# Optimization experiments

Hardware: AMD Instinct MI355X
Metric: run time of the kernel (lower is better)

## Reference

```python
import jax, jax.numpy as jnp
import numpy as np

T_MAX = 0.5
LN_EPS = 1e-5
B, N, D = 256, 16384, 512
NNZ = N * 33  # ~ (2*top_k+1) nonzeros per row of the sparse Laplacian
DF = 4 * D
DT = 32  # time-embedding hidden size


def _layernorm(x, g, b):
    mu = jnp.mean(x, axis=-1, keepdims=True)
    var = jnp.mean((x - mu) ** 2, axis=-1, keepdims=True)
    return (x - mu) * jax.lax.rsqrt(var + LN_EPS) * g + b


def setup_inputs() -> dict:
    key = jax.random.key(0)
    ks = jax.random.split(key, 16)

    def lin_w(k, fan_out, fan_in):
        return jax.random.normal(k, (fan_out, fan_in), jnp.float32) * (1.0 / np.sqrt(fan_in))

    inp = {}
    inp["x0"] = jax.random.uniform(ks[0], (B, N), jnp.float32)
    inp["t"] = jax.random.uniform(ks[1], (B,), jnp.float32)
    inp["L_vals"] = jax.random.normal(ks[2], (NNZ,), jnp.float32) * 0.1
    inp["W_in"] = lin_w(ks[3], D, N)
    inp["b_in"] = jnp.zeros((D,), jnp.float32)
    inp["W_out"] = lin_w(ks[4], N, D)
    inp["b_out"] = jnp.zeros((N,), jnp.float32)
    inp["W_qkv"] = lin_w(ks[5], 3 * D, D)
    inp["b_qkv"] = jnp.zeros((3 * D,), jnp.float32)
    inp["W_o"] = lin_w(ks[6], D, D)
    inp["b_o"] = jnp.zeros((D,), jnp.float32)
    inp["g1"] = jnp.ones((D,), jnp.float32)
    inp["be1"] = jnp.zeros((D,), jnp.float32)
    inp["g2"] = jnp.ones((D,), jnp.float32)
    inp["be2"] = jnp.zeros((D,), jnp.float32)
    inp["W_f1"] = lin_w(ks[7], DF, D)
    inp["b_f1"] = jnp.zeros((DF,), jnp.float32)
    inp["W_f2"] = lin_w(ks[8], D, DF)
    inp["b_f2"] = jnp.zeros((D,), jnp.float32)
    inp["W_t1"] = lin_w(ks[9], DT, 1)
    inp["b_t1"] = jnp.zeros((DT,), jnp.float32)
    inp["W_t2"] = lin_w(ks[10], D, DT)
    inp["b_t2"] = jnp.zeros((D,), jnp.float32)
    inp["L_rows"] = jax.random.randint(ks[11], (NNZ,), 0, N, jnp.int32)
    inp["L_cols"] = jax.random.randint(ks[12], (NNZ,), 0, N, jnp.int32)
    return inp


def reference(x0, t, L_vals, W_in, b_in, W_out, b_out, W_qkv, b_qkv, W_o, b_o,
              g1, be1, g2, be2, W_f1, b_f1, W_f2, b_f2, W_t1, b_t1, W_t2, b_t2,
              L_rows, L_cols):
    n_items = x0.shape[1]
    d_model = W_in.shape[0]
    t_cont = t * T_MAX  # per-sample diffusion time (explicit input, not RNG)

    # Batched sparse Laplacian diffusion (replaces the per-row torch.sparse.mm loop):
    # (L @ x.T)[i, b] = sum_e L_vals[e] * x0[b, L_cols[e]] aggregated to row L_rows[e]
    contrib = x0[:, L_cols] * L_vals                                  # (B, NNZ)
    Lx = jax.ops.segment_sum(contrib.T, L_rows, num_segments=n_items)  # (N, B)
    x_t = x0 - t_cont[:, None] * Lx.T                                  # (B, N)

    # Denoiser (eval mode: dropout off)
    h = x_t @ W_in.T + b_in                                            # (B, D)
    t_norm = t_cont / T_MAX
    te = jax.nn.silu(t_norm[:, None] @ W_t1.T + b_t1) @ W_t2.T + b_t2  # (B, D)
    h = h + te

    # MultiheadAttention on a length-1 sequence: softmax over one key is exactly 1,
    # so attn_out = out_proj(V) with V = h @ W_v.T + b_v.
    qkv = h @ W_qkv.T + b_qkv                                          # (B, 3D)
    v = qkv[:, 2 * d_model:]
    attn_out = v @ W_o.T + b_o

    h = _layernorm(h + attn_out, g1, be1)
    ff = jax.nn.gelu(h @ W_f1.T + b_f1, approximate=False) @ W_f2.T + b_f2
    h = _layernorm(h + ff, g2, be2)

    pred = h @ W_out.T + b_out                                         # (B, N)
    return jnp.mean((pred - x0) ** 2)
```

## Files before the change

### kernel.cpp

```cpp
#include <hip/hip_runtime.h>
#include <math.h>

#define Bb   256
#define Nn   16384
#define Dd   512
#define NNZn 540672
#define DFf  2048
#define SLOT 64

#define CVT_BLKS 4736
#define TR_BLKS  1024
#define BK_BLKS  2112
#define PREP_BLKS (CVT_BLKS + TR_BLKS + BK_BLKS)

#define C1 65536
#define C2 131072
#define C3 393216
#define C4 655360
#define C5 2752512
#define C6 4849664

typedef __bf16 bf16;
typedef __bf16 bf16x4 __attribute__((ext_vector_type(4)));
typedef __bf16 bf16x8 __attribute__((ext_vector_type(8)));
typedef float  f32x4  __attribute__((ext_vector_type(4)));

__device__ __forceinline__ void gload16(const void* g, void* l) {
  __builtin_amdgcn_global_load_lds(
      (const __attribute__((address_space(1))) unsigned int*)g,
      (__attribute__((address_space(3))) unsigned int*)l, 16, 0, 0);
}

template <int NK>
__device__ __forceinline__ void bar_keep() {
  asm volatile("s_waitcnt vmcnt(%0) lgkmcnt(0)" :: "n"(NK) : "memory");
  __builtin_amdgcn_s_barrier();
}

__device__ __forceinline__ float f16_of(unsigned e) {
  unsigned short us = (unsigned short)(e & 0xffff);
  _Float16 h;
  __builtin_memcpy(&h, &us, 2);
  return (float)h;
}

__global__ __launch_bounds__(256) void k_prep(
    const float* __restrict__ w_v, const float* __restrict__ w_o,
    const float* __restrict__ w_f1, const float* __restrict__ w_f2,
    const float* __restrict__ w_in, const float* __restrict__ w_out,
    bf16* __restrict__ o_v, bf16* __restrict__ o_o,
    bf16* __restrict__ o_f1, bf16* __restrict__ o_f2,
    bf16* __restrict__ o_in, bf16* __restrict__ o_out,
    const float* __restrict__ x0, bf16* __restrict__ x0T,
    const int* __restrict__ rows, const int* __restrict__ cols,
    const float* __restrict__ vals,
    int* __restrict__ counts, unsigned* __restrict__ ents,
    float* __restrict__ d_loss) {
  __shared__ float tile[64][65];
  int blk = blockIdx.x;
  if (blk == 0 && threadIdx.x == 0) *d_loss = 0.f;
  int q = blk / 3;
  if ((blk % 3) == 0 && q < BK_BLKS) {
    int i = q * 256 + threadIdx.x;
    int r = rows[i];
    int p = atomicAdd(&counts[r], 1);
    if (p < SLOT) {
      _Float16 hv = (_Float16)vals[i];
      unsigned short us;
      __builtin_memcpy(&us, &hv, 2);
      ents[(size_t)r * SLOT + p] = ((unsigned)cols[i] << 16) | (unsigned)us;
    }
  } else {
    int sB = (blk + 2) / 3; if (sB > BK_BLKS) sB = BK_BLKS;
    int o = blk - sB;
    if (o < CVT_BLKS) {
      int v0i = o * 1024 + threadIdx.x;
#pragma unroll
      for (int j = 0; j < 4; j++) {
        int v = v0i + j * 256;
        const float* s; bf16* d; int base;
        if (v < C2)      { if (v < C1) { s = w_v;  d = o_v;  base = 0;  }
                           else        { s = w_o;  d = o_o;  base = C1; } }
        else if (v < C4) { if (v < C3) { s = w_f1; d = o_f1; base = C2; }
                           else        { s = w_f2; d = o_f2; base = C3; } }
        else             { if (v < C5) { s = w_in; d = o_in; base = C4; }
                           else        { s = w_out; d = o_out; base = C5; } }
        int idx = (v - base) * 4;
        float4 x = *(const float4*)(s + idx);
        bf16x4 ob;
        ob[0] = (bf16)x.x; ob[1] = (bf16)x.y; ob[2] = (bf16)x.z; ob[3] = (bf16)x.w;
        *(bf16x4*)(d + idx) = ob;
      }
    } else {
      int bx = o - CVT_BLKS;
      int n0 = (bx & 255) * 64, b0 = (bx >> 8) * 64;
      int tx = threadIdx.x & 63, ty = threadIdx.x >> 6;
#pragma unroll
      for (int i = 0; i < 16; i++) {
        int bl = ty * 16 + i;
        tile[bl][tx] = x0[(size_t)(b0 + bl) * Nn + n0 + tx];
      }
      __syncthreads();
#pragma unroll
      for (int i = 0; i < 16; i++) {
        int nl = ty * 16 + i;
        x0T[(size_t)(n0 + nl) * Bb + b0 + tx] = (bf16)tile[tx][nl];
      }
    }
  }
}

__global__ __launch_bounds__(256) void k_lx(const bf16x4* __restrict__ x0T4,
                                            const int* __restrict__ counts,
                                            const unsigned* __restrict__ ents,
                                            bf16x4* __restrict__ Lx4) {
  int w = threadIdx.x >> 6, lane = threadIdx.x & 63;
  int r = blockIdx.x * 4 + w;
  __shared__ unsigned esm[4][64];
  int cnt = counts[r];
  if (cnt > SLOT) cnt = SLOT;
  const unsigned* ep = ents + (size_t)r * SLOT;
  float a0 = 0.f, a1 = 0.f, a2 = 0.f, a3 = 0.f;
  float b0 = 0.f, b1 = 0.f, b2 = 0.f, b3 = 0.f;
  float c0 = 0.f, c1 = 0.f, c2 = 0.f, c3 = 0.f;
  float d0 = 0.f, d1 = 0.f, d2 = 0.f, d3 = 0.f;
  for (int base = 0; base < cnt; base += 64) {
    int m = cnt - base; if (m > 64) m = 64;
    if (lane < m) esm[w][lane] = ep[base + lane];
    int i = 0;
    for (; i + 3 < m; i += 4) {
      unsigned e0 = esm[w][i],     e1 = esm[w][i + 1];
      unsigned e2 = esm[w][i + 2], e3 = esm[w][i + 3];
      bf16x4 xv0 = x0T4[(size_t)(e0 >> 16) * 64 + lane];
      bf16x4 xv1 = x0T4[(size_t)(e1 >> 16) * 64 + lane];
      bf16x4 xv2 = x0T4[(size_t)(e2 >> 16) * 64 + lane];
      bf16x4 xv3 = x0T4[(size_t)(e3 >> 16) * 64 + lane];
      float v0 = f16_of(e0), v1 = f16_of(e1), v2 = f16_of(e2), v3 = f16_of(e3);
      a0 += v0 * (float)xv0[0]; a1 += v0 * (float)xv0[1];
      a2 += v0 * (float)xv0[2]; a3 += v0 * (float)xv0[3];
      b0 += v1 * (float)xv1[0]; b1 += v1 * (float)xv1[1];
      b2 += v1 * (float)xv1[2]; b3 += v1 * (float)xv1[3];
      c0 += v2 * (float)xv2[0]; c1 += v2 * (float)xv2[1];
      c2 += v2 * (float)xv2[2]; c3 += v2 * (float)xv2[3];
      d0 += v3 * (float)xv3[0]; d1 += v3 * (float)xv3[1];
      d2 += v3 * (float)xv3[2]; d3 += v3 * (float)xv3[3];
    }
    for (; i < m; i++) {
      unsigned e0 = esm[w][i];
      bf16x4 xv0 = x0T4[(size_t)(e0 >> 16) * 64 + lane];
      float v0 = f16_of(e0);
      a0 += v0 * (float)xv0[0]; a1 += v0 * (float)xv0[1];
      a2 += v0 * (float)xv0[2]; a3 += v0 * (float)xv0[3];
    }
  }
  bf16x4 o;
  o[0] = (bf16)(a0 + b0 + c0 + d0); o[1] = (bf16)(a1 + b1 + c1 + d1);
  o[2] = (bf16)(a2 + b2 + c2 + d2); o[3] = (bf16)(a3 + b3 + c3 + d3);
  Lx4[(size_t)r * 64 + lane] = o;
}

__global__ __launch_bounds__(256) void k_combine(const float* __restrict__ x0,
                                                 const bf16* __restrict__ Lx,
                                                 const float* __restrict__ t,
                                                 bf16* __restrict__ xt) {
  __shared__ float lxs[64][65];
  int n0 = blockIdx.x * 64, b0 = blockIdx.y * 64;
  int tx = threadIdx.x & 63, ty = threadIdx.x >> 6;
#pragma unroll
  for (int i = 0; i < 16; i++) {
    int nl = ty * 16 + i;
    lxs[nl][tx] = (float)Lx[(size_t)(n0 + nl) * Bb + b0 + tx];
  }
  __syncthreads();
#pragma unroll
  for (int i = 0; i < 16; i++) {
    int bl = ty * 16 + i;
    int b  = b0 + bl;
    float tc = t[b] * 0.5f;
    float v = x0[(size_t)b * Nn + n0 + tx] - tc * lxs[tx][bl];
    xt[(size_t)b * Nn + n0 + tx] = (bf16)v;
  }
}

template <int BM, int BN, int MODE, int ACT = 0>
__global__ __launch_bounds__(256) void gemm_tn(
    const bf16* __restrict__ A, const bf16* __restrict__ Bm,
    float* __restrict__ C, int N, int K, int kLen, int MN,
    const float* __restrict__ bias, const float* __restrict__ x0,
    float* __restrict__ lossOut) {
  constexpr int WM = BM / 2, WN = BN / 2, FM = WM / 16, FN = WN / 16;
  constexpr int PASS = (BM + BN) / 64;
  constexpr int KEEP = PASS;
  __shared__ __align__(16) bf16 As[3][BM * 32];
  __shared__ __align__(16) bf16 Bs[3][BN * 32];
  __shared__ float lred[4];
  const int tid = threadIdx.x;
  const int lane = tid & 63, w = tid >> 6;
  const int wm = w >> 1, wn = w & 1;
  const int mBase = blockIdx.x * BM, nBase = blockIdx.y * BN;
  const int k0 = blockIdx.z * kLen;
  const int nIter = kLen >> 5;

  f32x4 acc[FM][FN];
#pragma unroll
  for (int i = 0; i < FM; i++)
#pragma unroll
    for (int j = 0; j < FN; j++) acc[i][j] = {0.f, 0.f, 0.f, 0.f};

  auto stage = [&](int buf, int k) {
#pragma unroll
    for (int p = 0; p < PASS; p++) {
      int c = p * 4 + w;
      int u = c * 64 + lane;
      if (c < BM / 16) {
        int row = u >> 2, sub = u & 3;
        gload16(A + (size_t)(mBase + row) * K + k + sub * 8,
                (char*)As[buf] + c * 1024);
      } else {
        int u2 = u - BM * 4;
        int row = u2 >> 2, sub = u2 & 3;
        gload16(Bm + (size_t)(nBase + row) * K + k + sub * 8,
                (char*)Bs[buf] + (c - BM / 16) * 1024);
      }
    }
  };
  auto compute = [&](int cur) {
    bf16x8 af[FM], bfr[FN];
#pragma unroll
    for (int i = 0; i < FM; i++)
      af[i] = *(const bf16x8*)(As[cur] + (wm * WM + i * 16 + (lane & 15)) * 32 + (lane >> 4) * 8);
#pragma unroll
    for (int j = 0; j < FN; j++)
      bfr[j] = *(const bf16x8*)(Bs[cur] + (wn * WN + j * 16 + (lane & 15)) * 32 + (lane >> 4) * 8);
#pragma unroll
    for (int i = 0; i < FM; i++)
#pragma unroll
      for (int j = 0; j < FN; j++)
        acc[i][j] = __builtin_amdgcn_mfma_f32_16x16x32_bf16(af[i], bfr[j], acc[i][j], 0, 0, 0);
  };

  stage(0, k0);
  if (nIter > 1) {
    stage(1, k0 + 32);
    bar_keep<KEEP>();
  } else {
    bar_keep<0>();
  }

  int c0 = 0, c1 = 1, c2 = 2;
  for (int t = 0; t < nIter; t += 2) {
    {
      const bool more2 = (t + 2 < nIter);
      if (more2) stage(c2, k0 + (t + 2) * 32);
      compute(c0);
      if (more2) bar_keep<KEEP>(); else bar_keep<0>();
    }
    {
      const bool more3 = (t + 3 < nIter);
      if (more3) stage(c0, k0 + (t + 3) * 32);
      compute(c1);
      if (more3) bar_keep<KEEP>(); else bar_keep<0>();
    }
    int tmp = c2; c2 = c1; c1 = c0; c0 = tmp;
  }

  if constexpr (MODE == 0) {
    float* Cz = C + (size_t)blockIdx.z * MN;
#pragma unroll
    for (int i = 0; i < FM; i++)
#pragma unroll
      for (int j = 0; j < FN; j++) {
        int n  = nBase + wn * WN + j * 16 + (lane & 15);
        int mB = mBase + wm * WM + i * 16 + ((lane >> 4) << 2);
#pragma unroll
        for (int r = 0; r < 4; r++)
          Cz[(size_t)(mB + r) * N + n] = acc[i][j][r];
      }
  } else if constexpr (MODE == 1) {
    bf16* Cb = (bf16*)C;
#pragma unroll
    for (int i = 0; i < FM; i++)
#pragma unroll
      for (int j = 0; j < FN; j++) {
        int n  = nBase + wn * WN + j * 16 + (lane & 15);
        float bo = bias[n];
        int mB = mBase + wm * WM + i * 16 + ((lane >> 4) << 2);
#pragma unroll
        for (int r = 0; r < 4; r++) {
          float x = acc[i][j][r] + bo;
          if constexpr (ACT == 1)
            x = 0.5f * x * (1.f + erff(x * 0.70710678118654752f));
          Cb[(size_t)(mB + r) * N + n] = (bf16)x;
        }
      }
  } else {
    float lsum = 0.f;
#pragma unroll
    for (int i = 0; i < FM; i++)
#pragma unroll
      for (int j = 0; j < FN; j++) {
        int n  = nBase + wn * WN + j * 16 + (lane & 15);
        float bo = bias[n];
        int mB = mBase + wm * WM + i * 16 + ((lane >> 4) << 2);
#pragma unroll
        for (int r = 0; r < 4; r++) {
          float d = acc[i][j][r] + bo - x0[(size_t)(mB + r) * N + n];
          lsum += d * d;
        }
      }
    for (int off = 32; off > 0; off >>= 1) lsum += __shfl_down(lsum, off, 64);
    if (lane == 0) lred[w] = lsum;
    __syncthreads();
    if (tid == 0)
      atomicAdd(lossOut,
                (lred[0] + lred[1] + lred[2] + lred[3]) * (1.f / 4194304.f));
  }
}

__global__ __launch_bounds__(512) void k_epi_h(const float* __restrict__ P,
                                               const float* __restrict__ t,
                                               const float* __restrict__ W_t1,
                                               const float* __restrict__ b_t1,
                                               const float* __restrict__ W_t2,
                                               const float* __restrict__ b_t2,
                                               const float* __restrict__ b_in,
                                               float* __restrict__ h_f32,
                                               bf16* __restrict__ h_b) {
  int b = blockIdx.x, d = threadIdx.x;
  __shared__ float s[32];
  if (d < 32) {
    float z = t[b] * W_t1[d] + b_t1[d];
    s[d] = z / (1.f + expf(-z));
  }
  __syncthreads();
  int i = b * Dd + d;
  float v = b_in[d] + b_t2[d];
#pragma unroll
  for (int sp = 0; sp < 32; sp++) v += P[sp * (Bb * Dd) + i];
#pragma unroll
  for (int j = 0; j < 32; j++) v += s[j] * W_t2[d * 32 + j];
  h_f32[i] = v;
  h_b[i] = (bf16)v;
}

template <int NS>
__global__ __launch_bounds__(512) void k_ln(const float* __restrict__ base,
                                            const float* __restrict__ add,
                                            const float* __restrict__ bias,
                                            const float* __restrict__ g,
                                            const float* __restrict__ be,
                                            float* __restrict__ out_f32,
                                            bf16* __restrict__ out_b) {
  int b = blockIdx.x, d = threadIdx.x;
  __shared__ float red[16];
  int i = b * Dd + d;
  float x = base[i] + bias[d];
#pragma unroll
  for (int sp = 0; sp < NS; sp++) x += add[sp * (Bb * Dd) + i];
  int w = d >> 6, lane = d & 63;
  float s = x;
  for (int off = 32; off > 0; off >>= 1) s += __shfl_down(s, off, 64);
  if (lane == 0) red[w] = s;
  __syncthreads();
  if (d == 0) {
    float tot = 0.f;
    for (int q = 0; q < 8; q++) tot += red[q];
    red[8] = tot * (1.f / 512.f);
  }
  __syncthreads();
  float mu = red[8];
  float c = x - mu;
  float s2 = c * c;
  for (int off = 32; off > 0; off >>= 1) s2 += __shfl_down(s2, off, 64);
  if (lane == 0) red[w] = s2;
  __syncthreads();
  if (d == 0) {
    float tot = 0.f;
    for (int q = 0; q < 8; q++) tot += red[q];
    red[8] = tot * (1.f / 512.f);
  }
  __syncthreads();
  float var = red[8];
  float y = c * rsqrtf(var + 1e-5f) * g[d] + be[d];
  if (out_f32) out_f32[i] = y;
  out_b[i] = (bf16)y;
}

extern "C" void kernel_launch(void* const* d_in, const int* in_sizes, int n_in,
                              void* d_out, int out_size, void* d_ws, size_t ws_size,
                              hipStream_t stream) {
  const float* x0    = (const float*)d_in[0];
  const float* t     = (const float*)d_in[1];
  const float* Lv    = (const float*)d_in[2];
  const float* W_in  = (const float*)d_in[3];
  const float* b_in  = (const float*)d_in[4];
  const float* W_out = (const float*)d_in[5];
  const float* b_out = (const float*)d_in[6];
  const float* W_qkv = (const float*)d_in[7];
  const float* b_qkv = (const float*)d_in[8];
  const float* W_o   = (const float*)d_in[9];
  const float* b_o   = (const float*)d_in[10];
  const float* g1    = (const float*)d_in[11];
  const float* be1   = (const float*)d_in[12];
  const float* g2    = (const float*)d_in[13];
  const float* be2   = (const float*)d_in[14];
  const float* W_f1  = (const float*)d_in[15];
  const float* b_f1  = (const float*)d_in[16];
  const float* W_f2  = (const float*)d_in[17];
  const float* b_f2  = (const float*)d_in[18];
  const float* W_t1  = (const float*)d_in[19];
  const float* b_t1  = (const float*)d_in[20];
  const float* W_t2  = (const float*)d_in[21];
  const float* b_t2  = (const float*)d_in[22];
  const int* L_rows  = (const int*)d_in[23];
  const int* L_cols  = (const int*)d_in[24];

  size_t off = 0;
  char* ws = (char*)d_ws;
  auto carve = [&](size_t bytes) -> void* {
    void* p = ws + off;
    off += (bytes + 255) & ~(size_t)255;
    return p;
  };

  bf16* W_v_b    = (bf16*)carve((size_t)Dd * Dd * 2);
  bf16* W_o_b    = (bf16*)carve((size_t)Dd * Dd * 2);
  bf16* W_f1_b   = (bf16*)carve((size_t)DFf * Dd * 2);
  bf16* W_f2_b   = (bf16*)carve((size_t)Dd * DFf * 2);
  bf16* W_in_b   = (bf16*)carve((size_t)Dd * Nn * 2);
  bf16* W_out_b  = (bf16*)carve((size_t)Nn * Dd * 2);
  bf16* x0T_b    = (bf16*)carve((size_t)Nn * Bb * 2);
  bf16* Lx_b     = (bf16*)carve((size_t)Nn * Bb * 2);
  bf16* xt_b     = (bf16*)carve((size_t)Bb * Nn * 2);
  float* p_h     = (float*)carve((size_t)32 * Bb * Dd * 4);
  float* p_at    = (float*)carve((size_t)Bb * Dd * 4);
  float* p_f2    = (float*)carve((size_t)4 * Bb * Dd * 4);
  float* h_f32   = (float*)carve((size_t)Bb * Dd * 4);
  bf16* h_b      = (bf16*)carve((size_t)Bb * Dd * 2);
  bf16* v_b      = (bf16*)carve((size_t)Bb * Dd * 2);
  float* hln_f32 = (float*)carve((size_t)Bb * Dd * 4);
  bf16* hln_b    = (bf16*)carve((size_t)Bb * Dd * 2);
  bf16* f1_b     = (bf16*)carve((size_t)Bb * DFf * 2);
  bf16* h2_b     = (bf16*)carve((size_t)Bb * Dd * 2);
  int* counts    = (int*)carve((size_t)Nn * 4);
  unsigned* ents = (unsigned*)carve((size_t)Nn * SLOT * 4);
  (void)in_sizes; (void)n_in; (void)out_size; (void)ws_size; (void)Lv;

  hipMemsetAsync(counts, 0, (size_t)Nn * 4, stream);

  k_prep<<<PREP_BLKS, 256, 0, stream>>>(
      W_qkv + (size_t)2 * Dd * Dd, W_o, W_f1, W_f2, W_in, W_out,
      W_v_b, W_o_b, W_f1_b, W_f2_b, W_in_b, W_out_b,
      x0, x0T_b, L_rows, L_cols, Lv, counts, ents, (float*)d_out);

  k_lx<<<Nn / 4, 256, 0, stream>>>((const bf16x4*)x0T_b, counts, ents,
                                   (bf16x4*)Lx_b);
  k_combine<<<dim3(256, 4), 256, 0, stream>>>(x0, Lx_b, t, xt_b);

  gemm_tn<128, 64, 0><<<dim3(2, 8, 32), 256, 0, stream>>>(
      xt_b, W_in_b, p_h, Dd, Nn, 512, Bb * Dd, nullptr, nullptr, nullptr);
  k_epi_h<<<Bb, 512, 0, stream>>>(p_h, t, W_t1, b_t1, W_t2, b_t2, b_in, h_f32, h_b);

  gemm_tn<32, 32, 1><<<dim3(8, 16, 1), 256, 0, stream>>>(
      h_b, W_v_b, (float*)v_b, Dd, Dd, 512, 0, b_qkv + 2 * Dd, nullptr, nullptr);

  gemm_tn<32, 32, 0><<<dim3(8, 16, 1), 256, 0, stream>>>(
      v_b, W_o_b, p_at, Dd, Dd, 512, 0, nullptr, nullptr, nullptr);
  k_ln<1><<<Bb, 512, 0, stream>>>(h_f32, p_at, b_o, g1, be1, hln_f32, hln_b);

  gemm_tn<32, 32, 1, 1><<<dim3(8, 64, 1), 256, 0, stream>>>(
      hln_b, W_f1_b, (float*)f1_b, DFf, Dd, 512, 0, b_f1, nullptr, nullptr);

  gemm_tn<32, 32, 0><<<dim3(8, 16, 4), 256, 0, stream>>>(
      f1_b, W_f2_b, p_f2, Dd, DFf, 512, Bb * Dd, nullptr, nullptr, nullptr);
  k_ln<4><<<Bb, 512, 0, stream>>>(hln_f32, p_f2, b_f2, g2, be2, nullptr, h2_b);

  gemm_tn<128, 64, 2><<<dim3(2, 256, 1), 256, 0, stream>>>(
      h2_b, W_out_b, nullptr, Nn, Dd, 512, 0, b_out, x0, (float*)d_out);
}
```

Before: 284.9 us.

## Move W_out bf16 conversion into idle blocks of small attention GEMMs

The fp32-to-bf16 conversion of W_out (8M elements) is taken out of the big prep kernel and split across extra blocks appended to the grids of the two small 512x512 V and out-projection GEMMs. Those GEMMs use only 128 blocks each and leave the GPU mostly idle, so the conversion bandwidth is meant to overlap with them instead of lengthening the prep kernel, which is on the critical path. The prep kernel's block interleaving ratio is changed from 1:2 to 1:1 to match the smaller conversion count. The risk is that the extra blocks delay the latency-bound small GEMMs.

```diff
diff --git a/kernel.cpp b/kernel.cpp
--- a/kernel.cpp
+++ b/kernel.cpp
@@ -8,7 +8,7 @@
 #define DFf  2048
 #define SLOT 64
 
-#define CVT_BLKS 4736
+#define CVT_BLKS 2688
 #define TR_BLKS  1024
 #define BK_BLKS  2112
 #define PREP_BLKS (CVT_BLKS + TR_BLKS + BK_BLKS)
@@ -18,7 +18,7 @@
 #define C3 393216
 #define C4 655360
 #define C5 2752512
-#define C6 4849664
+#define WOUT_VEC4 2097152
 
 typedef __bf16 bf16;
 typedef __bf16 bf16x4 __attribute__((ext_vector_type(4)));
@@ -47,10 +47,10 @@
 __global__ __launch_bounds__(256) void k_prep(
     const float* __restrict__ w_v, const float* __restrict__ w_o,
     const float* __restrict__ w_f1, const float* __restrict__ w_f2,
-    const float* __restrict__ w_in, const float* __restrict__ w_out,
+    const float* __restrict__ w_in,
     bf16* __restrict__ o_v, bf16* __restrict__ o_o,
     bf16* __restrict__ o_f1, bf16* __restrict__ o_f2,
-    bf16* __restrict__ o_in, bf16* __restrict__ o_out,
+    bf16* __restrict__ o_in,
     const float* __restrict__ x0, bf16* __restrict__ x0T,
     const int* __restrict__ rows, const int* __restrict__ cols,
     const float* __restrict__ vals,
@@ -59,8 +59,8 @@
   __shared__ float tile[64][65];
   int blk = blockIdx.x;
   if (blk == 0 && threadIdx.x == 0) *d_loss = 0.f;
-  int q = blk / 3;
-  if ((blk % 3) == 0 && q < BK_BLKS) {
+  int q = blk >> 1;
+  if (!(blk & 1) && q < BK_BLKS) {
     int i = q * 256 + threadIdx.x;
     int r = rows[i];
     int p = atomicAdd(&counts[r], 1);
@@ -71,7 +71,7 @@
       ents[(size_t)r * SLOT + p] = ((unsigned)cols[i] << 16) | (unsigned)us;
     }
   } else {
-    int sB = (blk + 2) / 3; if (sB > BK_BLKS) sB = BK_BLKS;
+    int sB = (blk + 1) >> 1; if (sB > BK_BLKS) sB = BK_BLKS;
     int o = blk - sB;
     if (o < CVT_BLKS) {
       int v0i = o * 1024 + threadIdx.x;
@@ -83,8 +83,7 @@
                            else        { s = w_o;  d = o_o;  base = C1; } }
         else if (v < C4) { if (v < C3) { s = w_f1; d = o_f1; base = C2; }
                            else        { s = w_f2; d = o_f2; base = C3; } }
-        else             { if (v < C5) { s = w_in; d = o_in; base = C4; }
-                           else        { s = w_out; d = o_out; base = C5; } }
+        else             { s = w_in; d = o_in; base = C4; }
         int idx = (v - base) * 4;
         float4 x = *(const float4*)(s + idx);
         bf16x4 ob;
@@ -182,12 +181,28 @@
   }
 }
 
-template <int BM, int BN, int MODE, int ACT = 0>
+template <int BM, int BN, int MODE, int ACT = 0, int GY = 0>
 __global__ __launch_bounds__(256) void gemm_tn(
     const bf16* __restrict__ A, const bf16* __restrict__ Bm,
     float* __restrict__ C, int N, int K, int kLen, int MN,
     const float* __restrict__ bias, const float* __restrict__ x0,
-    float* __restrict__ lossOut) {
+    float* __restrict__ lossOut,
+    const float* __restrict__ cvs, bf16* __restrict__ cvd, int cvoff) {
+  if constexpr (GY > 0) {
+    if (blockIdx.y >= GY) {
+      int cb = (blockIdx.y - GY) * gridDim.x + blockIdx.x;
+      int v0 = cvoff + cb * 1024 + threadIdx.x;
+#pragma unroll
+      for (int j = 0; j < 4; j++) {
+        int v = v0 + j * 256;
+        float4 x = *(const float4*)(cvs + (size_t)v * 4);
+        bf16x4 ob;
+        ob[0] = (bf16)x.x; ob[1] = (bf16)x.y; ob[2] = (bf16)x.z; ob[3] = (bf16)x.w;
+        *(bf16x4*)(cvd + (size_t)v * 4) = ob;
+      }
+      return;
+    }
+  }
   constexpr int WM = BM / 2, WN = BN / 2, FM = WM / 16, FN = WN / 16;
   constexpr int PASS = (BM + BN) / 64;
   constexpr int KEEP = PASS;
@@ -449,8 +464,8 @@
   hipMemsetAsync(counts, 0, (size_t)Nn * 4, stream);
 
   k_prep<<<PREP_BLKS, 256, 0, stream>>>(
-      W_qkv + (size_t)2 * Dd * Dd, W_o, W_f1, W_f2, W_in, W_out,
-      W_v_b, W_o_b, W_f1_b, W_f2_b, W_in_b, W_out_b,
+      W_qkv + (size_t)2 * Dd * Dd, W_o, W_f1, W_f2, W_in,
+      W_v_b, W_o_b, W_f1_b, W_f2_b, W_in_b,
       x0, x0T_b, L_rows, L_cols, Lv, counts, ents, (float*)d_out);
 
   k_lx<<<Nn / 4, 256, 0, stream>>>((const bf16x4*)x0T_b, counts, ents,
@@ -458,23 +473,29 @@
   k_combine<<<dim3(256, 4), 256, 0, stream>>>(x0, Lx_b, t, xt_b);
 
   gemm_tn<128, 64, 0><<<dim3(2, 8, 32), 256, 0, stream>>>(
-      xt_b, W_in_b, p_h, Dd, Nn, 512, Bb * Dd, nullptr, nullptr, nullptr);
+      xt_b, W_in_b, p_h, Dd, Nn, 512, Bb * Dd, nullptr, nullptr, nullptr,
+      nullptr, nullptr, 0);
   k_epi_h<<<Bb, 512, 0, stream>>>(p_h, t, W_t1, b_t1, W_t2, b_t2, b_in, h_f32, h_b);
 
-  gemm_tn<32, 32, 1><<<dim3(8, 16, 1), 256, 0, stream>>>(
-      h_b, W_v_b, (float*)v_b, Dd, Dd, 512, 0, b_qkv + 2 * Dd, nullptr, nullptr);
-
-  gemm_tn<32, 32, 0><<<dim3(8, 16, 1), 256, 0, stream>>>(
-      v_b, W_o_b, p_at, Dd, Dd, 512, 0, nullptr, nullptr, nullptr);
+  gemm_tn<32, 32, 1, 0, 16><<<dim3(8, 16 + 128, 1), 256, 0, stream>>>(
+      h_b, W_v_b, (float*)v_b, Dd, Dd, 512, 0, b_qkv + 2 * Dd, nullptr, nullptr,
+      W_out, W_out_b, 0);
+
+  gemm_tn<32, 32, 0, 0, 16><<<dim3(8, 16 + 128, 1), 256, 0, stream>>>(
+      v_b, W_o_b, p_at, Dd, Dd, 512, 0, nullptr, nullptr, nullptr,
+      W_out, W_out_b, WOUT_VEC4 / 2);
   k_ln<1><<<Bb, 512, 0, stream>>>(h_f32, p_at, b_o, g1, be1, hln_f32, hln_b);
 
   gemm_tn<32, 32, 1, 1><<<dim3(8, 64, 1), 256, 0, stream>>>(
-      hln_b, W_f1_b, (float*)f1_b, DFf, Dd, 512, 0, b_f1, nullptr, nullptr);
+      hln_b, W_f1_b, (float*)f1_b, DFf, Dd, 512, 0, b_f1, nullptr, nullptr,
+      nullptr, nullptr, 0);
 
   gemm_tn<32, 32, 0><<<dim3(8, 16, 4), 256, 0, stream>>>(
-      f1_b, W_f2_b, p_f2, Dd, DFf, 512, Bb * Dd, nullptr, nullptr, nullptr);
+      f1_b, W_f2_b, p_f2, Dd, DFf, 512, Bb * Dd, nullptr, nullptr, nullptr,
+      nullptr, nullptr, 0);
   k_ln<4><<<Bb, 512, 0, stream>>>(hln_f32, p_f2, b_f2, g2, be2, nullptr, h2_b);
 
   gemm_tn<128, 64, 2><<<dim3(2, 256, 1), 256, 0, stream>>>(
-      h2_b, W_out_b, nullptr, Nn, Dd, 512, 0, b_out, x0, (float*)d_out);
-}
+      h2_b, W_out_b, nullptr, Nn, Dd, 512, 0, b_out, x0, (float*)d_out,
+      nullptr, nullptr, 0);
+}
```

New measurement: 290.8 us. 2.1% more time.
